# Performance work log

Measured on AMD Instinct MI355X. Metric: run time of the kernel, lower is better.

Reference implementation:

```python
import jax, jax.numpy as jnp
import numpy as np

BETA = 0.25  # qtz_beta


def setup_inputs() -> dict:
    key = jax.random.key(0)
    kz, kc = jax.random.split(key)
    N, D, K = 131072, 256, 1024
    z = jax.random.normal(kz, (N, D), dtype=jnp.float32)
    # torch init: uniform(-1/latent_dim, 1/latent_dim)
    codebook = jax.random.uniform(kc, (K, D), dtype=jnp.float32,
                                  minval=-1.0 / D, maxval=1.0 / D)
    return {"z": z, "codebook": codebook}


def reference(z, codebook):
    # pairwise squared distances: ||z||^2 - 2 z C^T + ||C||^2  -> [N, K]
    d = (jnp.sum(z * z, axis=-1, keepdims=True)
         - 2.0 * jnp.einsum('nd,kd->nk', z, codebook)
         + jnp.sum(codebook * codebook, axis=-1)[None, :])
    min_embed_ids = jnp.argmin(d, axis=-1)          # [N] int
    z_q = codebook[min_embed_ids]                   # gather == one_hot @ codebook
    # codebook loss (hard path, calculate_loss=True)
    codebook_loss = (jnp.mean((jax.lax.stop_gradient(z_q) - z) ** 2)
                     + BETA * jnp.mean((z_q - jax.lax.stop_gradient(z)) ** 2))
    # straight-through estimator
    z_q_st = z + jax.lax.stop_gradient(z_q - z)
    return (z, z_q_st, min_embed_ids, codebook_loss)
```

## Files before the change

kernel.cpp:

```cpp
#include <hip/hip_runtime.h>

#define N_TOK 131072
#define DIM   256
#define KCB   1024

#define RT    128
#define KT    128
#define TAU   0.02f
#define EMIT_CAP 4096
#define CB_SCALE 4096.0f
#define ACC_SCL  4.8828125e-4f

typedef __attribute__((ext_vector_type(8))) _Float16 f16x8;
typedef __attribute__((ext_vector_type(4))) float f32x4;

__device__ __forceinline__ void gload_lds16(const short* g, short* l) {
  __builtin_amdgcn_global_load_lds(
      (const __attribute__((address_space(1))) void*)g,
      (__attribute__((address_space(3))) void*)l, 16, 0, 0);
}

__device__ __forceinline__ float np_sumsq_128(const float* __restrict__ p) {
#pragma clang fp contract(off)
  float4 a = *(const float4*)(p);
  float4 b = *(const float4*)(p + 4);
  float r0 = a.x * a.x, r1 = a.y * a.y, r2 = a.z * a.z, r3 = a.w * a.w;
  float r4 = b.x * b.x, r5 = b.y * b.y, r6 = b.z * b.z, r7 = b.w * b.w;
  for (int i = 8; i < 128; i += 8) {
    float4 c = *(const float4*)(p + i);
    float4 d = *(const float4*)(p + i + 4);
    r0 += c.x * c.x; r1 += c.y * c.y; r2 += c.z * c.z; r3 += c.w * c.w;
    r4 += d.x * d.x; r5 += d.y * d.y; r6 += d.z * d.z; r7 += d.w * d.w;
  }
  return ((r0 + r1) + (r2 + r3)) + ((r4 + r5) + (r6 + r7));
}

__global__ void prep_cc(const float* __restrict__ cb, float* __restrict__ cc,
                        double* __restrict__ loss_acc) {
  int k = blockIdx.x * blockDim.x + threadIdx.x;
  if (k == 0) *loss_acc = 0.0;
  if (k < KCB) {
    const float* p = cb + (long)k * DIM;
    cc[k] = np_sumsq_128(p) + np_sumsq_128(p + 128);
  }
}

__global__ void prep_h16(const float* __restrict__ cb, short* __restrict__ ch) {
  int o = blockIdx.x * blockDim.x + threadIdx.x;
  if (o < KCB * DIM) {
    int dl = o & 7, k15 = (o >> 3) & 15, qd = (o >> 7) & 3;
    int dsl = (o >> 9) & 1, kg8 = (o >> 10) & 7;
    int p = (o >> 13) & 3, kt = (o >> 15) & 7;
    int k = kt * 128 + kg8 * 16 + k15;
    int d = (2 * p + dsl) * 32 + qd * 8 + dl;
    float v = cb[k * DIM + d] * CB_SCALE;
    ((_Float16*)ch)[o] = (_Float16)v;
  }
}

__global__ __launch_bounds__(256, 3)
void argmin_kernel(const float* __restrict__ z, const float* __restrict__ cb,
                   const short* __restrict__ ch_g,
                   const float* __restrict__ cc_g, float* __restrict__ ids_f) {
  __shared__ __align__(16) short cbuf[2][8192];
  __shared__ float zz_s[RT];
  __shared__ float zz_half[RT][2];
  __shared__ unsigned rowmin_s[RT];
  __shared__ int kmin_s[RT];
  __shared__ unsigned emit_s[EMIT_CAP];
  __shared__ int emit_cnt;

  const int t    = threadIdx.x;
  const int lane = t & 63;
  const int w    = t >> 6;
  const int l15  = lane & 15;
  const int qd   = lane >> 4;
  const long rowbase = (long)blockIdx.x * RT;

#pragma unroll
  for (int j = 0; j < 4; ++j) {
    int off = w * 2048 + j * 512 + lane * 8;
    gload_lds16(ch_g + off, &cbuf[0][0] + off);
  }

  {
    int r = t >> 1, h = t & 1;
    zz_half[r][h] = np_sumsq_128(z + (rowbase + r) * DIM + h * 128);
  }
  if (t < RT) { rowmin_s[t] = 0xFFFFFFFFu; kmin_s[t] = 0x7FFFFFFF; }
  if (t == 0) emit_cnt = 0;

  f16x8 a16[2][8];
  {
    const float* zp0 = z + (rowbase + 32 * w + l15) * (long)DIM + qd * 8;
#pragma unroll
    for (int m = 0; m < 2; ++m) {
      const float* zp = zp0 + m * 16 * DIM;
#pragma unroll
      for (int ds = 0; ds < 8; ++ds) {
        float4 v0 = *(const float4*)(zp + ds * 32);
        float4 v1 = *(const float4*)(zp + ds * 32 + 4);
        float f[8] = {v0.x, v0.y, v0.z, v0.w, v1.x, v1.y, v1.z, v1.w};
#pragma unroll
        for (int j = 0; j < 8; ++j) a16[m][ds][j] = (_Float16)f[j];
      }
    }
  }

  __syncthreads();
  if (t < RT) zz_s[t] = zz_half[t][0] + zz_half[t][1];

#pragma clang loop unroll(disable)
  for (int kt = 0; kt < 8; ++kt) {
    f32x4 acc[2][8];
#pragma unroll
    for (int m = 0; m < 2; ++m)
#pragma unroll
      for (int c = 0; c < 8; ++c) acc[m][c] = (f32x4){0.f, 0.f, 0.f, 0.f};

#pragma unroll
    for (int p = 0; p < 4; ++p) {
      int s = kt * 4 + p;
      if (s < 31) {
        const short* src = ch_g + (long)(s + 1) * 8192;
#pragma unroll
        for (int j = 0; j < 4; ++j) {
          int off = w * 2048 + j * 512 + lane * 8;
          gload_lds16(src + off, &cbuf[(p + 1) & 1][0] + off);
        }
      }
#pragma unroll
      for (int dsl = 0; dsl < 2; ++dsl) {
#pragma unroll
        for (int c = 0; c < 8; ++c) {
          f16x8 b = *(const f16x8*)&cbuf[p & 1][c * 1024 + dsl * 512 + lane * 8];
          acc[0][c] = __builtin_amdgcn_mfma_f32_16x16x32_f16(a16[0][2 * p + dsl], b, acc[0][c], 0, 0, 0);
          acc[1][c] = __builtin_amdgcn_mfma_f32_16x16x32_f16(a16[1][2 * p + dsl], b, acc[1][c], 0, 0, 0);
        }
      }
      if (p < 3) __syncthreads();
    }

    float ccv[8];
#pragma unroll
    for (int c = 0; c < 8; ++c) ccv[c] = cc_g[kt * KT + 16 * c + l15];
    float rmin[2][4];
#pragma unroll
    for (int m = 0; m < 2; ++m)
#pragma unroll
      for (int rg = 0; rg < 4; ++rg) {
        int row = 32 * w + 16 * m + 4 * qd + rg;
        float zz = zz_s[row];
        float mn = __builtin_inff();
#pragma unroll
        for (int c = 0; c < 8; ++c) {
          float dv = (zz - acc[m][c][rg] * ACC_SCL) + ccv[c];
          mn = fminf(mn, dv);
        }
        rmin[m][rg] = mn;
      }
#pragma unroll
    for (int off = 1; off < 16; off <<= 1)
#pragma unroll
      for (int m = 0; m < 2; ++m)
#pragma unroll
        for (int rg = 0; rg < 4; ++rg)
          rmin[m][rg] = fminf(rmin[m][rg], __shfl_xor(rmin[m][rg], off, 64));
    if (l15 == 0) {
#pragma unroll
      for (int m = 0; m < 2; ++m)
#pragma unroll
        for (int rg = 0; rg < 4; ++rg)
          atomicMin(&rowmin_s[32 * w + 16 * m + 4 * qd + rg], __float_as_uint(rmin[m][rg]));
    }
    __syncthreads();
#pragma unroll
    for (int m = 0; m < 2; ++m)
#pragma unroll
      for (int rg = 0; rg < 4; ++rg) {
        int row = 32 * w + 16 * m + 4 * qd + rg;
        float th = __uint_as_float(rowmin_s[row]) + TAU;
        float zz = zz_s[row];
#pragma unroll
        for (int c = 0; c < 8; ++c) {
          int k = kt * KT + 16 * c + l15;
          float dv = (zz - acc[m][c][rg] * ACC_SCL) + ccv[c];
          if (dv <= th) {
            int idx = atomicAdd(&emit_cnt, 1);
            if (idx < EMIT_CAP) emit_s[idx] = ((unsigned)row << 10) | (unsigned)k;
          }
        }
      }
  }

  __syncthreads();
  int cnt = emit_cnt;
  bool over = cnt > EMIT_CAP;
  if (t < RT) rowmin_s[t] = 0xFFFFFFFFu;
  __syncthreads();

  if (!over) {
    unsigned mydd[16]; int myn[16], myk[16]; int mc = 0;
    for (int p = t; p < cnt; p += 256) {
      unsigned e = emit_s[p];
      int n = (int)(e >> 10), k = (int)(e & 1023);
      const float* zp = z + (rowbase + n) * DIM;
      const float* cp = cb + (long)k * DIM;
      float dot = 0.f;
      for (int d = 0; d < DIM; d += 4) {
        float4 zv = *(const float4*)(zp + d);
        float4 cv = *(const float4*)(cp + d);
        dot = fmaf(zv.x, cv.x, dot); dot = fmaf(zv.y, cv.y, dot);
        dot = fmaf(zv.z, cv.z, dot); dot = fmaf(zv.w, cv.w, dot);
      }
      float dd = (zz_s[n] - 2.0f * dot) + cc_g[k];
      mydd[mc] = __float_as_uint(dd); myn[mc] = n; myk[mc] = k; ++mc;
      atomicMin(&rowmin_s[n], __float_as_uint(dd));
    }
    __syncthreads();
    for (int i = 0; i < mc; ++i)
      if (mydd[i] == rowmin_s[myn[i]]) atomicMin(&kmin_s[myn[i]], myk[i]);
  } else {
    for (int p = t; p < RT * KCB; p += 256) {
      int n = p >> 10, k = p & 1023;
      const float* zp = z + (rowbase + n) * DIM;
      const float* cp = cb + (long)k * DIM;
      float dot = 0.f;
      for (int d = 0; d < DIM; d += 4) {
        float4 zv = *(const float4*)(zp + d);
        float4 cv = *(const float4*)(cp + d);
        dot = fmaf(zv.x, cv.x, dot); dot = fmaf(zv.y, cv.y, dot);
        dot = fmaf(zv.z, cv.z, dot); dot = fmaf(zv.w, cv.w, dot);
      }
      float dd = (zz_s[n] - 2.0f * dot) + cc_g[k];
      atomicMin(&rowmin_s[n], __float_as_uint(dd));
    }
    __syncthreads();
    for (int p = t; p < RT * KCB; p += 256) {
      int n = p >> 10, k = p & 1023;
      const float* zp = z + (rowbase + n) * DIM;
      const float* cp = cb + (long)k * DIM;
      float dot = 0.f;
      for (int d = 0; d < DIM; d += 4) {
        float4 zv = *(const float4*)(zp + d);
        float4 cv = *(const float4*)(cp + d);
        dot = fmaf(zv.x, cv.x, dot); dot = fmaf(zv.y, cv.y, dot);
        dot = fmaf(zv.z, cv.z, dot); dot = fmaf(zv.w, cv.w, dot);
      }
      float dd = (zz_s[n] - 2.0f * dot) + cc_g[k];
      if (__float_as_uint(dd) == rowmin_s[n]) atomicMin(&kmin_s[n], k);
    }
  }
  __syncthreads();
  if (t < RT) ids_f[rowbase + t] = (float)kmin_s[t];
}

__global__ void output_kernel(const float* __restrict__ z, const float* __restrict__ cb,
                              const float* __restrict__ ids_f,
                              float* __restrict__ out_z, float* __restrict__ out_zq,
                              double* __restrict__ loss_acc) {
  __shared__ double red[4];
  double acc = 0.0;
  const long total4 = (long)N_TOK * DIM / 4;
  long idx    = (long)blockIdx.x * blockDim.x + threadIdx.x;
  long stride = (long)gridDim.x * blockDim.x;
  for (long i = idx; i < total4; i += stride) {
    long e = i * 4;
    long r = e >> 8;
    int  k = (int)ids_f[r];
    float4 vz = *(const float4*)(z + e);
    float4 vc = *(const float4*)(cb + (long)k * DIM + (e & 255));
    *(float4*)(out_z + e)  = vz;
    *(float4*)(out_zq + e) = vc;
    float d0 = vc.x - vz.x, d1 = vc.y - vz.y, d2 = vc.z - vz.z, d3 = vc.w - vz.w;
    acc += (double)(d0 * d0) + (double)(d1 * d1) + (double)(d2 * d2) + (double)(d3 * d3);
  }
#pragma unroll
  for (int off = 32; off > 0; off >>= 1) acc += __shfl_down(acc, off, 64);
  int lane = threadIdx.x & 63, wv = threadIdx.x >> 6;
  if (lane == 0) red[wv] = acc;
  __syncthreads();
  if (threadIdx.x == 0) {
    double s = (red[0] + red[1]) + (red[2] + red[3]);
    atomicAdd(loss_acc, s);
  }
}

__global__ void finalize_kernel(const double* __restrict__ loss_acc,
                                float* __restrict__ out_loss) {
  if (threadIdx.x == 0) {
    double mean = *loss_acc / (double)((long)N_TOK * DIM);
    out_loss[0] = (float)(1.25 * mean);
  }
}

extern "C" void kernel_launch(void* const* d_in, const int* in_sizes, int n_in,
                              void* d_out, int out_size, void* d_ws, size_t ws_size,
                              hipStream_t stream) {
  const float* z  = (const float*)d_in[0];
  const float* cb = (const float*)d_in[1];
  float* out      = (float*)d_out;
  float* out_z    = out;
  float* out_zq   = out + (long)N_TOK * DIM;
  float* out_ids  = out_zq + (long)N_TOK * DIM;
  float* out_loss = out_ids + N_TOK;

  double* loss_acc = (double*)d_ws;

  short* ch_g = (short*)((char*)d_out);
  float* cc_g = (float*)((char*)d_out + 524288);

  prep_cc<<<4, 256, 0, stream>>>(cb, cc_g, loss_acc);
  prep_h16<<<KCB * DIM / 256, 256, 0, stream>>>(cb, ch_g);
  argmin_kernel<<<N_TOK / RT, 256, 0, stream>>>(z, cb, ch_g, cc_g, out_ids);
  output_kernel<<<2048, 256, 0, stream>>>(z, cb, out_ids, out_z, out_zq, loss_acc);
  finalize_kernel<<<1, 64, 0, stream>>>(loss_acc, out_loss);
}
```

Before: 770.7 us.

## Restructure VQ argmin with 256-row blocks, per-wave running-min candidates, packed atomics

The argmin kernel now uses 512-thread blocks over 256 rows. Each codebook stage is a 64KB tile loaded into LDS in one pass, with a sync before the next load instead of fine-grained double buffering. Codebook norms are kept in LDS, and the ||z||^2 term is dropped from the approximate screening. Each wave keeps a running per-row min and rechecks candidates exactly, stage by stage, through a small per-wave emit list. Those exact rechecks use 64-bit packed atomicMin into global memory, which removes the block-wide rowmin/kmin passes. The loss reduction moves to per-block slots with a tree finalize instead of a double atomic. The risks are less load/compute overlap, since the single buffer is not double-buffered, and repeated exact-distance recomputation, including ||z||^2, for every candidate.

```diff
diff --git a/kernel.cpp b/kernel.cpp
--- a/kernel.cpp
+++ b/kernel.cpp
@@ -4,10 +4,10 @@
 #define DIM   256
 #define KCB   1024
 
-#define RT    128
-#define KT    128
+#define RPB   256
+#define NSTG  8
 #define TAU   0.02f
-#define EMIT_CAP 4096
+#define ECAP  126
 #define CB_SCALE 4096.0f
 #define ACC_SCL  4.8828125e-4f
 
@@ -35,64 +35,73 @@
   return ((r0 + r1) + (r2 + r3)) + ((r4 + r5) + (r6 + r7));
 }
 
+__device__ __forceinline__ float exact_dd(const float* __restrict__ zp,
+                                          const float* __restrict__ cp,
+                                          float cc) {
+  float zz = np_sumsq_128(zp) + np_sumsq_128(zp + 128);
+  float dot = 0.f;
+  for (int d = 0; d < DIM; d += 4) {
+    float4 zv = *(const float4*)(zp + d);
+    float4 cv = *(const float4*)(cp + d);
+    dot = fmaf(zv.x, cv.x, dot); dot = fmaf(zv.y, cv.y, dot);
+    dot = fmaf(zv.z, cv.z, dot); dot = fmaf(zv.w, cv.w, dot);
+  }
+  return (zz - 2.0f * dot) + cc;
+}
+
 __global__ void prep_cc(const float* __restrict__ cb, float* __restrict__ cc,
-                        double* __restrict__ loss_acc) {
-  int k = blockIdx.x * blockDim.x + threadIdx.x;
-  if (k == 0) *loss_acc = 0.0;
-  if (k < KCB) {
-    const float* p = cb + (long)k * DIM;
-    cc[k] = np_sumsq_128(p) + np_sumsq_128(p + 128);
-  }
-}
-
-__global__ void prep_h16(const float* __restrict__ cb, short* __restrict__ ch) {
+                        double* __restrict__ slots, int nslots) {
+  int gid = blockIdx.x * blockDim.x + threadIdx.x;
+  for (int i = gid; i < nslots; i += 1024) slots[i] = 0.0;
+  if (gid < KCB) {
+    const float* p = cb + (long)gid * DIM;
+    cc[gid] = np_sumsq_128(p) + np_sumsq_128(p + 128);
+  }
+}
+
+__global__ void prep_h16(const float* __restrict__ cb, short* __restrict__ ch,
+                         unsigned long long* __restrict__ packed) {
   int o = blockIdx.x * blockDim.x + threadIdx.x;
+  if (o < N_TOK) packed[o] = ~0ull;
   if (o < KCB * DIM) {
     int dl = o & 7, k15 = (o >> 3) & 15, qd = (o >> 7) & 3;
-    int dsl = (o >> 9) & 1, kg8 = (o >> 10) & 7;
-    int p = (o >> 13) & 3, kt = (o >> 15) & 7;
-    int k = kt * 128 + kg8 * 16 + k15;
-    int d = (2 * p + dsl) * 32 + qd * 8 + dl;
+    int ds = (o >> 9) & 7, cf = (o >> 12) & 15, q = (o >> 16) & 3;
+    int k = q * 256 + cf * 16 + k15;
+    int d = ds * 32 + qd * 8 + dl;
     float v = cb[k * DIM + d] * CB_SCALE;
     ((_Float16*)ch)[o] = (_Float16)v;
   }
 }
 
-__global__ __launch_bounds__(256, 3)
-void argmin_kernel(const float* __restrict__ z, const float* __restrict__ cb,
-                   const short* __restrict__ ch_g,
-                   const float* __restrict__ cc_g, float* __restrict__ ids_f) {
-  __shared__ __align__(16) short cbuf[2][8192];
-  __shared__ float zz_s[RT];
-  __shared__ float zz_half[RT][2];
-  __shared__ unsigned rowmin_s[RT];
-  __shared__ int kmin_s[RT];
-  __shared__ unsigned emit_s[EMIT_CAP];
-  __shared__ int emit_cnt;
+__global__ __launch_bounds__(512, 2)
+void vq_kernel(const float* __restrict__ z, const float* __restrict__ cb,
+               const short* __restrict__ ch_g, const float* __restrict__ cc_g,
+               unsigned long long* __restrict__ packed) {
+  __shared__ __align__(16) short cbuf[32768];
+  __shared__ __align__(16) float cc_s[KCB];
+  __shared__ unsigned emit_s[8][ECAP + 2];
 
   const int t    = threadIdx.x;
   const int lane = t & 63;
-  const int w    = t >> 6;
+  const int wv   = t >> 6;
   const int l15  = lane & 15;
   const int qd   = lane >> 4;
-  const long rowbase = (long)blockIdx.x * RT;
-
-#pragma unroll
-  for (int j = 0; j < 4; ++j) {
-    int off = w * 2048 + j * 512 + lane * 8;
-    gload_lds16(ch_g + off, &cbuf[0][0] + off);
-  }
-
-  {
-    int r = t >> 1, h = t & 1;
-    zz_half[r][h] = np_sumsq_128(z + (rowbase + r) * DIM + h * 128);
-  }
-  if (t < RT) { rowmin_s[t] = 0xFFFFFFFFu; kmin_s[t] = 0x7FFFFFFF; }
-  if (t == 0) emit_cnt = 0;
+  const long rowbase = (long)blockIdx.x * RPB;
+
+#pragma unroll
+  for (int j = 0; j < 8; ++j) {
+    int off = wv * 4096 + j * 512 + lane * 8;
+    gload_lds16(ch_g + off, &cbuf[0] + off);
+  }
+  if (wv < 4) {
+    int off = wv * 512 + lane * 8;
+    gload_lds16((const short*)cc_g + off, (short*)cc_s + off);
+  }
+  if (lane == 0) emit_s[wv][0] = 0u;
 
   f16x8 a16[2][8];
   {
-    const float* zp0 = z + (rowbase + 32 * w + l15) * (long)DIM + qd * 8;
+    const float* zp0 = z + (rowbase + 32 * wv + l15) * (long)DIM + qd * 8;
 #pragma unroll
     for (int m = 0; m < 2; ++m) {
       const float* zp = zp0 + m * 16 * DIM;
@@ -107,58 +116,67 @@
     }
   }
 
+  float runmin[2][4];
+#pragma unroll
+  for (int m = 0; m < 2; ++m)
+#pragma unroll
+    for (int rg = 0; rg < 4; ++rg) runmin[m][rg] = __builtin_inff();
+
   __syncthreads();
-  if (t < RT) zz_s[t] = zz_half[t][0] + zz_half[t][1];
 
 #pragma clang loop unroll(disable)
-  for (int kt = 0; kt < 8; ++kt) {
+  for (int s = 0; s < NSTG; ++s) {
+    const int kbase = s * 128;
     f32x4 acc[2][8];
 #pragma unroll
     for (int m = 0; m < 2; ++m)
 #pragma unroll
       for (int c = 0; c < 8; ++c) acc[m][c] = (f32x4){0.f, 0.f, 0.f, 0.f};
-
-#pragma unroll
-    for (int p = 0; p < 4; ++p) {
-      int s = kt * 4 + p;
-      if (s < 31) {
-        const short* src = ch_g + (long)(s + 1) * 8192;
-#pragma unroll
-        for (int j = 0; j < 4; ++j) {
-          int off = w * 2048 + j * 512 + lane * 8;
-          gload_lds16(src + off, &cbuf[(p + 1) & 1][0] + off);
+#pragma unroll
+    for (int ds = 0; ds < 8; ++ds) {
+#pragma unroll
+      for (int c = 0; c < 8; ++c) {
+        f16x8 b = *(const f16x8*)&cbuf[(c * 8 + ds) * 512 + lane * 8];
+        acc[0][c] = __builtin_amdgcn_mfma_f32_16x16x32_f16(a16[0][ds], b, acc[0][c], 0, 0, 0);
+        acc[1][c] = __builtin_amdgcn_mfma_f32_16x16x32_f16(a16[1][ds], b, acc[1][c], 0, 0, 0);
+      }
+    }
+
+    __syncthreads();
+    if (s < NSTG - 1) {
+      const short* src = ch_g + (long)(s + 1) * 32768;
+#pragma unroll
+      for (int j = 0; j < 8; ++j) {
+        int off = wv * 4096 + j * 512 + lane * 8;
+        gload_lds16(src + off, &cbuf[0] + off);
+      }
+    }
+
+    float ccv[8];
+#pragma unroll
+    for (int c = 0; c < 8; ++c) ccv[c] = cc_s[kbase + 16 * c + l15];
+    float rmin[2][4];
+#pragma unroll
+    for (int m = 0; m < 2; ++m)
+#pragma unroll
+      for (int rg = 0; rg < 4; ++rg) rmin[m][rg] = __builtin_inff();
+
+#pragma unroll
+    for (int m = 0; m < 2; ++m)
+#pragma unroll
+      for (int c = 0; c < 8; ++c)
+#pragma unroll
+        for (int rg = 0; rg < 4; ++rg) {
+          float dv = fmaf(acc[m][c][rg], -ACC_SCL, ccv[c]);
+          if (s > 0 && dv <= runmin[m][rg] + TAU) {
+            unsigned idx = atomicAdd(&emit_s[wv][0], 1u);
+            if (idx < ECAP) {
+              unsigned row = (unsigned)(32 * wv + 16 * m + 4 * qd + rg);
+              emit_s[wv][1 + idx] = (row << 10) | (unsigned)(kbase + 16 * c + l15);
+            }
+          }
+          rmin[m][rg] = fminf(rmin[m][rg], dv);
         }
-      }
-#pragma unroll
-      for (int dsl = 0; dsl < 2; ++dsl) {
-#pragma unroll
-        for (int c = 0; c < 8; ++c) {
-          f16x8 b = *(const f16x8*)&cbuf[p & 1][c * 1024 + dsl * 512 + lane * 8];
-          acc[0][c] = __builtin_amdgcn_mfma_f32_16x16x32_f16(a16[0][2 * p + dsl], b, acc[0][c], 0, 0, 0);
-          acc[1][c] = __builtin_amdgcn_mfma_f32_16x16x32_f16(a16[1][2 * p + dsl], b, acc[1][c], 0, 0, 0);
-        }
-      }
-      if (p < 3) __syncthreads();
-    }
-
-    float ccv[8];
-#pragma unroll
-    for (int c = 0; c < 8; ++c) ccv[c] = cc_g[kt * KT + 16 * c + l15];
-    float rmin[2][4];
-#pragma unroll
-    for (int m = 0; m < 2; ++m)
-#pragma unroll
-      for (int rg = 0; rg < 4; ++rg) {
-        int row = 32 * w + 16 * m + 4 * qd + rg;
-        float zz = zz_s[row];
-        float mn = __builtin_inff();
-#pragma unroll
-        for (int c = 0; c < 8; ++c) {
-          float dv = (zz - acc[m][c][rg] * ACC_SCL) + ccv[c];
-          mn = fminf(mn, dv);
-        }
-        rmin[m][rg] = mn;
-      }
 #pragma unroll
     for (int off = 1; off < 16; off <<= 1)
 #pragma unroll
@@ -166,99 +184,62 @@
 #pragma unroll
         for (int rg = 0; rg < 4; ++rg)
           rmin[m][rg] = fminf(rmin[m][rg], __shfl_xor(rmin[m][rg], off, 64));
-    if (l15 == 0) {
+#pragma unroll
+    for (int m = 0; m < 2; ++m)
+#pragma unroll
+      for (int rg = 0; rg < 4; ++rg) runmin[m][rg] = fminf(runmin[m][rg], rmin[m][rg]);
+
+    if (s == 0) {
 #pragma unroll
       for (int m = 0; m < 2; ++m)
 #pragma unroll
-        for (int rg = 0; rg < 4; ++rg)
-          atomicMin(&rowmin_s[32 * w + 16 * m + 4 * qd + rg], __float_as_uint(rmin[m][rg]));
-    }
+        for (int c = 0; c < 8; ++c)
+#pragma unroll
+          for (int rg = 0; rg < 4; ++rg) {
+            float dv = fmaf(acc[m][c][rg], -ACC_SCL, ccv[c]);
+            if (dv <= runmin[m][rg] + TAU) {
+              unsigned idx = atomicAdd(&emit_s[wv][0], 1u);
+              if (idx < ECAP) {
+                unsigned row = (unsigned)(32 * wv + 16 * m + 4 * qd + rg);
+                emit_s[wv][1 + idx] = (row << 10) | (unsigned)(kbase + 16 * c + l15);
+              }
+            }
+          }
+    }
+
+    unsigned cnt = emit_s[wv][0];
+    if (cnt <= ECAP) {
+      for (unsigned p = (unsigned)lane; p < cnt; p += 64) {
+        unsigned e = emit_s[wv][1 + p];
+        int rl = (int)(e >> 10), k = (int)(e & 1023);
+        float dd = exact_dd(z + (rowbase + rl) * DIM, cb + (long)k * DIM, cc_s[k]);
+        atomicMin(&packed[rowbase + rl],
+                  ((unsigned long long)__float_as_uint(dd) << 32) | (unsigned)k);
+      }
+    } else {
+      for (int p = lane; p < 32 * 128; p += 64) {
+        int rl = 32 * wv + (p >> 7), k = kbase + (p & 127);
+        float dd = exact_dd(z + (rowbase + rl) * DIM, cb + (long)k * DIM, cc_s[k]);
+        atomicMin(&packed[rowbase + rl],
+                  ((unsigned long long)__float_as_uint(dd) << 32) | (unsigned)k);
+      }
+    }
+    if (lane == 0) emit_s[wv][0] = 0u;
+
     __syncthreads();
-#pragma unroll
-    for (int m = 0; m < 2; ++m)
-#pragma unroll
-      for (int rg = 0; rg < 4; ++rg) {
-        int row = 32 * w + 16 * m + 4 * qd + rg;
-        float th = __uint_as_float(rowmin_s[row]) + TAU;
-        float zz = zz_s[row];
-#pragma unroll
-        for (int c = 0; c < 8; ++c) {
-          int k = kt * KT + 16 * c + l15;
-          float dv = (zz - acc[m][c][rg] * ACC_SCL) + ccv[c];
-          if (dv <= th) {
-            int idx = atomicAdd(&emit_cnt, 1);
-            if (idx < EMIT_CAP) emit_s[idx] = ((unsigned)row << 10) | (unsigned)k;
-          }
-        }
-      }
-  }
-
-  __syncthreads();
-  int cnt = emit_cnt;
-  bool over = cnt > EMIT_CAP;
-  if (t < RT) rowmin_s[t] = 0xFFFFFFFFu;
-  __syncthreads();
-
-  if (!over) {
-    unsigned mydd[16]; int myn[16], myk[16]; int mc = 0;
-    for (int p = t; p < cnt; p += 256) {
-      unsigned e = emit_s[p];
-      int n = (int)(e >> 10), k = (int)(e & 1023);
-      const float* zp = z + (rowbase + n) * DIM;
-      const float* cp = cb + (long)k * DIM;
-      float dot = 0.f;
-      for (int d = 0; d < DIM; d += 4) {
-        float4 zv = *(const float4*)(zp + d);
-        float4 cv = *(const float4*)(cp + d);
-        dot = fmaf(zv.x, cv.x, dot); dot = fmaf(zv.y, cv.y, dot);
-        dot = fmaf(zv.z, cv.z, dot); dot = fmaf(zv.w, cv.w, dot);
-      }
-      float dd = (zz_s[n] - 2.0f * dot) + cc_g[k];
-      mydd[mc] = __float_as_uint(dd); myn[mc] = n; myk[mc] = k; ++mc;
-      atomicMin(&rowmin_s[n], __float_as_uint(dd));
-    }
-    __syncthreads();
-    for (int i = 0; i < mc; ++i)
-      if (mydd[i] == rowmin_s[myn[i]]) atomicMin(&kmin_s[myn[i]], myk[i]);
-  } else {
-    for (int p = t; p < RT * KCB; p += 256) {
-      int n = p >> 10, k = p & 1023;
-      const float* zp = z + (rowbase + n) * DIM;
-      const float* cp = cb + (long)k * DIM;
-      float dot = 0.f;
-      for (int d = 0; d < DIM; d += 4) {
-        float4 zv = *(const float4*)(zp + d);
-        float4 cv = *(const float4*)(cp + d);
-        dot = fmaf(zv.x, cv.x, dot); dot = fmaf(zv.y, cv.y, dot);
-        dot = fmaf(zv.z, cv.z, dot); dot = fmaf(zv.w, cv.w, dot);
-      }
-      float dd = (zz_s[n] - 2.0f * dot) + cc_g[k];
-      atomicMin(&rowmin_s[n], __float_as_uint(dd));
-    }
-    __syncthreads();
-    for (int p = t; p < RT * KCB; p += 256) {
-      int n = p >> 10, k = p & 1023;
-      const float* zp = z + (rowbase + n) * DIM;
-      const float* cp = cb + (long)k * DIM;
-      float dot = 0.f;
-      for (int d = 0; d < DIM; d += 4) {
-        float4 zv = *(const float4*)(zp + d);
-        float4 cv = *(const float4*)(cp + d);
-        dot = fmaf(zv.x, cv.x, dot); dot = fmaf(zv.y, cv.y, dot);
-        dot = fmaf(zv.z, cv.z, dot); dot = fmaf(zv.w, cv.w, dot);
-      }
-      float dd = (zz_s[n] - 2.0f * dot) + cc_g[k];
-      if (__float_as_uint(dd) == rowmin_s[n]) atomicMin(&kmin_s[n], k);
-    }
-  }
-  __syncthreads();
-  if (t < RT) ids_f[rowbase + t] = (float)kmin_s[t];
+  }
+}
+
+__global__ void extract_ids(const unsigned long long* __restrict__ packed,
+                            float* __restrict__ ids_f) {
+  int i = blockIdx.x * blockDim.x + threadIdx.x;
+  if (i < N_TOK) ids_f[i] = (float)(unsigned)(packed[i] & 0xFFFFFFFFull);
 }
 
 __global__ void output_kernel(const float* __restrict__ z, const float* __restrict__ cb,
                               const float* __restrict__ ids_f,
                               float* __restrict__ out_z, float* __restrict__ out_zq,
-                              double* __restrict__ loss_acc) {
+                              double* __restrict__ slots, int nslots) {
   __shared__ double red[4];
   double acc = 0.0;
   const long total4 = (long)N_TOK * DIM / 4;
@@ -277,20 +258,29 @@
   }
 #pragma unroll
   for (int off = 32; off > 0; off >>= 1) acc += __shfl_down(acc, off, 64);
-  int lane = threadIdx.x & 63, wv = threadIdx.x >> 6;
-  if (lane == 0) red[wv] = acc;
+  int lane = threadIdx.x & 63, wvv = threadIdx.x >> 6;
+  if (lane == 0) red[wvv] = acc;
+  __syncthreads();
+  if (threadIdx.x == 0) {
+    double sum = (red[0] + red[1]) + (red[2] + red[3]);
+    if (nslots > 1) slots[blockIdx.x] = sum;
+    else atomicAdd(&slots[0], sum);
+  }
+}
+
+__global__ void finalize_kernel(const double* __restrict__ slots, int nslots,
+                                float* __restrict__ out_loss) {
+  __shared__ double red[4];
+  double a = 0.0;
+  for (int i = threadIdx.x; i < nslots; i += 256) a += slots[i];
+#pragma unroll
+  for (int off = 32; off > 0; off >>= 1) a += __shfl_down(a, off, 64);
+  int lane = threadIdx.x & 63, wvv = threadIdx.x >> 6;
+  if (lane == 0) red[wvv] = a;
   __syncthreads();
   if (threadIdx.x == 0) {
     double s = (red[0] + red[1]) + (red[2] + red[3]);
-    atomicAdd(loss_acc, s);
-  }
-}
-
-__global__ void finalize_kernel(const double* __restrict__ loss_acc,
-                                float* __restrict__ out_loss) {
-  if (threadIdx.x == 0) {
-    double mean = *loss_acc / (double)((long)N_TOK * DIM);
-    out_loss[0] = (float)(1.25 * mean);
+    out_loss[0] = (float)(1.25 * (s / (double)((long)N_TOK * DIM)));
   }
 }
 
@@ -305,14 +295,17 @@
   float* out_ids  = out_zq + (long)N_TOK * DIM;
   float* out_loss = out_ids + N_TOK;
 
-  double* loss_acc = (double*)d_ws;
+  int nslots = (ws_size >= 2048 * sizeof(double)) ? 2048 : 1;
+  double* slots = (double*)d_ws;
 
   short* ch_g = (short*)((char*)d_out);
   float* cc_g = (float*)((char*)d_out + 524288);
-
-  prep_cc<<<4, 256, 0, stream>>>(cb, cc_g, loss_acc);
-  prep_h16<<<KCB * DIM / 256, 256, 0, stream>>>(cb, ch_g);
-  argmin_kernel<<<N_TOK / RT, 256, 0, stream>>>(z, cb, ch_g, cc_g, out_ids);
-  output_kernel<<<2048, 256, 0, stream>>>(z, cb, out_ids, out_z, out_zq, loss_acc);
-  finalize_kernel<<<1, 64, 0, stream>>>(loss_acc, out_loss);
-}
+  unsigned long long* packed = (unsigned long long*)((char*)d_out + 2097152);
+
+  prep_cc<<<4, 256, 0, stream>>>(cb, cc_g, slots, nslots);
+  prep_h16<<<KCB * DIM / 256, 256, 0, stream>>>(cb, ch_g, packed);
+  vq_kernel<<<N_TOK / RPB, 512, 0, stream>>>(z, cb, ch_g, cc_g, packed);
+  extract_ids<<<N_TOK / 256, 256, 0, stream>>>(packed, out_ids);
+  output_kernel<<<2048, 256, 0, stream>>>(z, cb, out_ids, out_z, out_zq, slots, nslots);
+  finalize_kernel<<<1, 256, 0, stream>>>(slots, nslots, out_loss);
+}
```

After: 1.159 ms. 1.5x slower.
